# Performance work log

Hardware: AMD Instinct MI355X
Metric: run time of the kernel (lower is better)

The kernel has to match this reference:

```python
import jax, jax.numpy as jnp
import numpy as np

K = 16  # number of neighbors (self excluded), matches init k
NUM_CLASSES = 100


def setup_inputs() -> dict:
    key = jax.random.key(0)
    kx, ky = jax.random.split(key)
    N, D = 8192, 256
    x = jax.random.normal(kx, (N, D), dtype=jnp.float32)
    y = jax.random.randint(ky, (N,), 0, NUM_CLASSES, dtype=jnp.int64)
    return {"x": x, "y": y}


def _knn_loss(x, y):
    N = x.shape[0]
    k = min(K, N - 1)
    # Pairwise squared Euclidean distances via Gram trick: [N, N]
    sq_norms = jnp.sum(x * x, axis=1)
    sq = sq_norms[:, None] + sq_norms[None, :] - 2.0 * (x @ x.T)
    sq = jnp.maximum(sq, 0.0)
    eye = jnp.eye(N, dtype=bool)
    # Keep sqrt grad-safe on the (excluded) diagonal by placing a dummy 1.0 there.
    d = jnp.sqrt(jnp.where(eye, 1.0, sq))  # [N, N] Euclidean distances

    # k nearest neighbors excluding self (BallTree query k+1 then drop col 0).
    d_for_knn = jnp.where(eye, jnp.inf, d)
    _, nn_idx = jax.lax.top_k(-d_for_knn, k)  # [N, k] indices of smallest distances

    # distances = exp(-d); denominator sums over all j != i.
    exp_d = jnp.where(eye, 0.0, jnp.exp(-d))
    denom = jnp.sum(exp_d, axis=1)  # [N]

    # log(exp(-d_in) / denom_i) = -d_in - log(denom_i)
    nn_d = jnp.take_along_axis(d, nn_idx, axis=1)          # [N, k]
    log_p = -nn_d - jnp.log(denom)[:, None]                 # [N, k]

    # Only neighbors with matching label contribute; rows with none are skipped.
    match = (y[nn_idx] == y[:, None]).astype(x.dtype)       # [N, k]
    cnt = jnp.sum(match, axis=1)                            # [N]
    row_mean = jnp.where(cnt > 0, jnp.sum(log_p * match, axis=1) / jnp.maximum(cnt, 1.0), 0.0)
    return -jnp.sum(row_mean) / N


def reference(x, y):
    return _knn_loss(x, y)
```

## Files before the change

kernel.cpp:

```cpp
#include <hip/hip_runtime.h>
#include <hip/hip_fp16.h>


typedef __attribute__((ext_vector_type(8))) short s8v;
typedef __attribute__((ext_vector_type(4))) float f32x4;

#define NROW 8192
#define NK   256
#define SAMPN 512
#define TAUR  6
#define PSLOT 2

template <bool B> struct BoolC { static constexpr bool value = B; };

#define OFF_DNP  0
#define OFF_NRM  262144
#define OFF_TAU  294912
#define OFF_XB   327680
#define OFF_SAMP 4521984
#define OFF_PASS 4521984
#define PASS_BYTES (NROW * 512 * 4)

__device__ __forceinline__ unsigned short f2bf(float f) {
  unsigned u = __float_as_uint(f);
  return (unsigned short)((u + 0x7FFFu + ((u >> 16) & 1u)) >> 16);
}

__device__ __forceinline__ void gld16(const void* g, void* l) {
  __builtin_amdgcn_global_load_lds(
      (const __attribute__((address_space(1))) unsigned int*)g,
      (__attribute__((address_space(3))) unsigned int*)l, 16, 0, 0);
}

__device__ __forceinline__ unsigned umin32(unsigned a, unsigned b) { return a < b ? a : b; }

__global__ __launch_bounds__(256) void k_prep(const float* __restrict__ x,
                                              unsigned short* __restrict__ xb,
                                              float* __restrict__ nrm) {
  const int w = threadIdx.x >> 6, l = threadIdx.x & 63;
  const int r = blockIdx.x * 4 + w;
  const float4 xv = *reinterpret_cast<const float4*>(x + r * NK + l * 4);
  float ns = xv.x * xv.x + xv.y * xv.y + xv.z * xv.z + xv.w * xv.w;
  ns += __shfl_xor(ns, 1);  ns += __shfl_xor(ns, 2);  ns += __shfl_xor(ns, 4);
  ns += __shfl_xor(ns, 8);  ns += __shfl_xor(ns, 16); ns += __shfl_xor(ns, 32);
  if (l == 0) nrm[r] = ns;
  ushort4 bv;
  bv.x = f2bf(xv.x); bv.y = f2bf(xv.y); bv.z = f2bf(xv.z); bv.w = f2bf(xv.w);
  const int gs = (l >> 1) ^ (r & 7);
  *reinterpret_cast<ushort4*>(xb + r * NK + gs * 8 + (l & 1) * 4) = bv;
}

__global__ __launch_bounds__(512) void k_samp(const unsigned short* __restrict__ xb,
                                              const float* __restrict__ nrm,
                                              unsigned short* __restrict__ samp) {
  __shared__ __align__(16) unsigned short Bl[64 * NK];
  __shared__ float ncs[64];
  const int tid = threadIdx.x;
  const int w = tid >> 6, l = tid & 63, l15 = l & 15, l4 = l >> 4;
  const int rb = blockIdx.x >> 3, ss = blockIdx.x & 7;
  const int rowbase = rb * 128 + (w >> 1) * 32;
  const int wcol = (w & 1) * 32;

  #pragma unroll
  for (int jj = 0; jj < 4; ++jj) {
    const int unit = jj * 512 + tid;
    const int sc = unit >> 5, gsl = unit & 31;
    const int s = ss * 64 + sc;
    const int jrow = s * 16 + (s & 7);
    gld16(xb + jrow * NK + gsl * 8, &Bl[unit * 8]);
  }
  if (tid < 64) {
    const int s = ss * 64 + tid;
    ncs[tid] = nrm[s * 16 + (s & 7)];
  }

  s8v A[2][8];
  #pragma unroll
  for (int rf = 0; rf < 2; ++rf) {
    const int rr = rowbase + rf * 16 + l15;
    #pragma unroll
    for (int kf = 0; kf < 8; ++kf) {
      const int g = ((kf << 2) | l4) ^ (rr & 7);
      A[rf][kf] = *reinterpret_cast<const s8v*>(xb + rr * NK + g * 8);
    }
  }
  float nr[2][4];
  #pragma unroll
  for (int rf = 0; rf < 2; ++rf)
    #pragma unroll
    for (int q = 0; q < 4; ++q) nr[rf][q] = nrm[rowbase + rf * 16 + l4 * 4 + q];

  __syncthreads();
  f32x4 acc[2][2];
  #pragma unroll
  for (int rf = 0; rf < 2; ++rf) {
    f32x4 z = {0.f, 0.f, 0.f, 0.f};
    acc[rf][0] = z; acc[rf][1] = z;
  }
  #pragma unroll
  for (int kf = 0; kf < 8; ++kf) {
    const int gs = ((kf << 2) | l4) ^ (l15 & 7);
    const s8v b0 = *reinterpret_cast<const s8v*>(&Bl[(wcol + l15) * NK + gs * 8]);
    const s8v b1 = *reinterpret_cast<const s8v*>(&Bl[(wcol + 16 + l15) * NK + gs * 8]);
    #pragma unroll
    for (int rf = 0; rf < 2; ++rf) {
      acc[rf][0] = __builtin_amdgcn_mfma_f32_16x16x32_bf16(A[rf][kf], b0, acc[rf][0], 0, 0, 0);
      acc[rf][1] = __builtin_amdgcn_mfma_f32_16x16x32_bf16(A[rf][kf], b1, acc[rf][1], 0, 0, 0);
    }
  }
  #pragma unroll
  for (int rf = 0; rf < 2; ++rf)
    #pragma unroll
    for (int cf = 0; cf < 2; ++cf) {
      const int scol = ss * 64 + wcol + cf * 16 + l15;
      const int jcol = scol * 16 + (scol & 7);
      const float nc = ncs[wcol + cf * 16 + l15];
      #pragma unroll
      for (int q = 0; q < 4; ++q) {
        const int rowg = rowbase + rf * 16 + l4 * 4 + q;
        const float sq = fmaxf(fmaf(acc[rf][cf][q], -2.0f, nr[rf][q] + nc), 0.0f);
        const float dd = __builtin_amdgcn_sqrtf(sq);
        unsigned short d16 = __half_as_ushort(__float2half(dd));
        if (jcol == rowg) d16 = 0xFFFFu;
        samp[rowg * SAMPN + scol] = d16;
      }
    }
}

__global__ __launch_bounds__(256) void k_tau(const unsigned short* __restrict__ samp,
                                             unsigned* __restrict__ tauk) {
  const int w = threadIdx.x >> 6, l = threadIdx.x & 63;
  const int r = blockIdx.x * 4 + w;
  const uint4 pa = *reinterpret_cast<const uint4*>(samp + r * SAMPN + l * 8);
  unsigned v[8];
  v[0] = pa.x & 0xFFFFu; v[1] = pa.x >> 16; v[2] = pa.y & 0xFFFFu; v[3] = pa.y >> 16;
  v[4] = pa.z & 0xFFFFu; v[5] = pa.z >> 16; v[6] = pa.w & 0xFFFFu; v[7] = pa.w >> 16;
  unsigned m = 0;
  for (int pp = 0; pp < TAUR; ++pp) {
    unsigned lm = v[0];
    #pragma unroll
    for (int j = 1; j < 8; ++j) lm = umin32(lm, v[j]);
    m = lm;
    m = umin32(m, __shfl_xor(m, 1));  m = umin32(m, __shfl_xor(m, 2));
    m = umin32(m, __shfl_xor(m, 4));  m = umin32(m, __shfl_xor(m, 8));
    m = umin32(m, __shfl_xor(m, 16)); m = umin32(m, __shfl_xor(m, 32));
    const unsigned long long bal = __ballot(lm == m);
    const int owner = (int)__ffsll(bal) - 1;
    if (l == owner) {
      bool f = false;
      #pragma unroll
      for (int j = 0; j < 8; ++j)
        if (!f && v[j] == m) { v[j] = 0xFFFFFFFFu; f = true; }
    }
  }
  if (l == 0) tauk[r] = m;
}

__global__ __launch_bounds__(512) void k_main(const unsigned short* __restrict__ xb,
                                              const float* __restrict__ nrm,
                                              const unsigned* __restrict__ tauk,
                                              float* __restrict__ dnp,
                                              unsigned* __restrict__ pass) {
  __shared__ __align__(16) unsigned short Bl[2][64 * NK];
  __shared__ float ncs[2][64];
  __shared__ float dpart[128];
  const int tid = threadIdx.x;
  const int w = tid >> 6, l = tid & 63, l15 = l & 15, l4 = l >> 4;
  const int rb = blockIdx.x >> 3, cs = blockIdx.x & 7;
  const int rowbase = rb * 128 + (w >> 1) * 32;
  const int wcol = (w & 1) * 32;
  const int colslice = cs * 1024;
  const unsigned long long ltm = (1ull << l) - 1ull;
  const unsigned long long sub = 0xFFFFull << (l4 * 16);

  if (tid < 128) dpart[tid] = 0.0f;

  s8v A[2][8];
  #pragma unroll
  for (int rf = 0; rf < 2; ++rf) {
    const int rr = rowbase + rf * 16 + l15;
    #pragma unroll
    for (int kf = 0; kf < 8; ++kf) {
      const int g = ((kf << 2) | l4) ^ (rr & 7);
      A[rf][kf] = *reinterpret_cast<const s8v*>(xb + rr * NK + g * 8);
    }
  }
  float nr[2][4], tk2[2][4], dn[2][4];
  #pragma unroll
  for (int rf = 0; rf < 2; ++rf)
    #pragma unroll
    for (int q = 0; q < 4; ++q) {
      const int rowg = rowbase + rf * 16 + l4 * 4 + q;
      nr[rf][q] = nrm[rowg];
      const float tw = __half2float(__ushort_as_half((unsigned short)(tauk[rowg] + 1u)));
      tk2[rf][q] = tw * tw;
      dn[rf][q] = 0.0f;
    }

  auto stage = [&](int buf, int t) {
    const unsigned short* src = xb + (colslice + t * 64) * NK;
    #pragma unroll
    for (int jj = 0; jj < 4; ++jj)
      gld16(src + (jj * 512 + tid) * 8, &Bl[buf][(jj * 512 + w * 64) * 8]);
    if (tid < 64) ncs[buf][tid] = nrm[colslice + t * 64 + tid];
  };

  const int tdiag = rb * 2 - cs * 16;

  stage(0, 0);
  for (int t = 0; t < 16; ++t) {
    const int cur = t & 1;
    __syncthreads();
    if (t + 1 < 16) stage(cur ^ 1, t + 1);
    const int cbase = colslice + t * 64;
    f32x4 acc[2][2];
    #pragma unroll
    for (int rf = 0; rf < 2; ++rf) {
      f32x4 z = {0.f, 0.f, 0.f, 0.f};
      acc[rf][0] = z; acc[rf][1] = z;
    }
    #pragma unroll
    for (int kf = 0; kf < 8; ++kf) {
      const int gs = ((kf << 2) | l4) ^ (l15 & 7);
      const s8v b0 = *reinterpret_cast<const s8v*>(&Bl[cur][(wcol + l15) * NK + gs * 8]);
      const s8v b1 = *reinterpret_cast<const s8v*>(&Bl[cur][(wcol + 16 + l15) * NK + gs * 8]);
      #pragma unroll
      for (int rf = 0; rf < 2; ++rf) {
        acc[rf][0] = __builtin_amdgcn_mfma_f32_16x16x32_bf16(A[rf][kf], b0, acc[rf][0], 0, 0, 0);
        acc[rf][1] = __builtin_amdgcn_mfma_f32_16x16x32_bf16(A[rf][kf], b1, acc[rf][1], 0, 0, 0);
      }
    }
    const float nc0 = ncs[cur][wcol + l15];
    const float nc1 = ncs[cur][wcol + 16 + l15];
    const int colg0 = cbase + wcol + l15;
    const int colg1 = colg0 + 16;
    const int gt4 = (cs * 16 + t) * 4;
    auto epi = [&](auto dgc) {
      constexpr bool DG = decltype(dgc)::value;
      #pragma unroll
      for (int rf = 0; rf < 2; ++rf)
        #pragma unroll
        for (int q = 0; q < 4; ++q) {
          const int rowg = rowbase + rf * 16 + l4 * 4 + q;
          float sq0 = fmaf(acc[rf][0][q], -2.0f, nr[rf][q] + nc0);
          float sq1 = fmaf(acc[rf][1][q], -2.0f, nr[rf][q] + nc1);
          if (DG) { sq0 = fmaxf(sq0, 0.0f); sq1 = fmaxf(sq1, 0.0f); }
          const float d0 = __builtin_amdgcn_sqrtf(sq0);
          const float d1 = __builtin_amdgcn_sqrtf(sq1);
          float e0 = __expf(-d0), e1 = __expf(-d1);
          bool p0 = sq0 < tk2[rf][q];
          bool p1 = sq1 < tk2[rf][q];
          if (DG) {
            const bool nd0 = (rowg != colg0), nd1 = (rowg != colg1);
            e0 = nd0 ? e0 : 0.0f;  e1 = nd1 ? e1 : 0.0f;
            p0 = p0 && nd0;  p1 = p1 && nd1;
          }
          dn[rf][q] += e0 + e1;
          const unsigned long long m0 = __ballot(p0);
          const unsigned long long m1 = __ballot(p1);
          if ((m0 | m1) != 0ull) {
            const int r0 = __popcll(m0 & sub & ltm);
            const int r1 = __popcll(m1 & sub & ltm);
            if (p0 && r0 < PSLOT) {
              const unsigned d16 = __half_as_ushort(__float2half(d0));
              pass[rowg * 512 + gt4 + r0] = (d16 << 16) | (unsigned)colg0;
            }
            if (p1 && r1 < PSLOT) {
              const unsigned d16 = __half_as_ushort(__float2half(d1));
              pass[rowg * 512 + gt4 + 2 + r1] = (d16 << 16) | (unsigned)colg1;
            }
          }
        }
    };
    if (t == tdiag || t == tdiag + 1) epi(BoolC<true>{});
    else                              epi(BoolC<false>{});
  }
  #pragma unroll
  for (int rf = 0; rf < 2; ++rf)
    #pragma unroll
    for (int q = 0; q < 4; ++q) {
      float vs = dn[rf][q];
      vs += __shfl_xor(vs, 1); vs += __shfl_xor(vs, 2);
      vs += __shfl_xor(vs, 4); vs += __shfl_xor(vs, 8);
      if (l15 == 0) atomicAdd(&dpart[(w >> 1) * 32 + rf * 16 + l4 * 4 + q], vs);
    }
  __syncthreads();
  if (tid < 128) dnp[(rb * 128 + tid) * 8 + cs] = dpart[tid];
}

__global__ __launch_bounds__(256) void k_fin(const unsigned* __restrict__ pass,
                                             const float* __restrict__ dnp,
                                             const int* __restrict__ y,
                                             float* __restrict__ out) {
  const int w = threadIdx.x >> 6, l = threadIdx.x & 63;
  const int r = blockIdx.x * 4 + w;
  unsigned kk[8];
  const uint4 pa = *reinterpret_cast<const uint4*>(pass + r * 512 + l * 8);
  const uint4 pb = *reinterpret_cast<const uint4*>(pass + r * 512 + l * 8 + 4);
  kk[0] = pa.x; kk[1] = pa.y; kk[2] = pa.z; kk[3] = pa.w;
  kk[4] = pb.x; kk[5] = pb.y; kk[6] = pb.z; kk[7] = pb.w;
  unsigned myKey = 0xFFFFFFFFu;
  for (int pp = 0; pp < 16; ++pp) {
    unsigned lm = kk[0];
    #pragma unroll
    for (int j = 1; j < 8; ++j) lm = umin32(lm, kk[j]);
    unsigned m = lm;
    m = umin32(m, __shfl_xor(m, 1));  m = umin32(m, __shfl_xor(m, 2));
    m = umin32(m, __shfl_xor(m, 4));  m = umin32(m, __shfl_xor(m, 8));
    m = umin32(m, __shfl_xor(m, 16)); m = umin32(m, __shfl_xor(m, 32));
    const unsigned long long bal = __ballot(lm == m);
    const int owner = (int)__ffsll(bal) - 1;
    if (l == owner) {
      bool f = false;
      #pragma unroll
      for (int j = 0; j < 8; ++j)
        if (!f && kk[j] == m) { kk[j] = 0xFFFFFFFFu; f = true; }
    }
    if (l == pp) myKey = m;
  }
  float den = 0.0f;
  #pragma unroll
  for (int cs = 0; cs < 8; ++cs) den += dnp[r * 8 + cs];
  const float logden = __logf(den);
  float contrib = 0.0f, cmf = 0.0f;
  if (l < 16 && myKey != 0xFFFFFFFFu) {
    const int col = (int)(myKey & 0x1FFFu);
    const float dd = __half2float(__ushort_as_half((unsigned short)(myKey >> 16)));
    if (y[col] == y[r]) { contrib = -dd - logden; cmf = 1.0f; }
  }
  contrib += __shfl_xor(contrib, 1);  contrib += __shfl_xor(contrib, 2);
  contrib += __shfl_xor(contrib, 4);  contrib += __shfl_xor(contrib, 8);
  contrib += __shfl_xor(contrib, 16); contrib += __shfl_xor(contrib, 32);
  cmf += __shfl_xor(cmf, 1);  cmf += __shfl_xor(cmf, 2);
  cmf += __shfl_xor(cmf, 4);  cmf += __shfl_xor(cmf, 8);
  cmf += __shfl_xor(cmf, 16); cmf += __shfl_xor(cmf, 32);
  if (l == 0 && cmf > 0.0f)
    atomicAdd(out, (contrib / cmf) * (-1.0f / 8192.0f));
}

extern "C" void kernel_launch(void* const* d_in, const int* in_sizes, int n_in,
                              void* d_out, int out_size, void* d_ws, size_t ws_size,
                              hipStream_t stream) {
  const float* x = (const float*)d_in[0];
  const int* y = (const int*)d_in[1];
  float* out = (float*)d_out;
  char* ws = (char*)d_ws;

  float*          dnp  = (float*)(ws + OFF_DNP);
  float*          nrm  = (float*)(ws + OFF_NRM);
  unsigned*       tauk = (unsigned*)(ws + OFF_TAU);
  unsigned short* xb   = (unsigned short*)(ws + OFF_XB);
  unsigned short* samp = (unsigned short*)(ws + OFF_SAMP);
  unsigned*       pass = (unsigned*)(ws + OFF_PASS);

  k_prep<<<2048, 256, 0, stream>>>(x, xb, nrm);
  k_samp<<<512,  512, 0, stream>>>(xb, nrm, samp);
  k_tau <<<2048, 256, 0, stream>>>(samp, tauk);
  hipMemsetAsync(pass, 0xFF, PASS_BYTES, stream);
  hipMemsetAsync(d_out, 0, sizeof(float), stream);
  k_main<<<512,  512, 0, stream>>>(xb, nrm, tauk, dnp, pass);
  k_fin <<<2048, 256, 0, stream>>>(pass, dnp, y, out);
}
```

Before: 133.6 us.

## Retile main kernel to 256-thread blocks over 32-column tiles with 16 column slices

The main distance kernel moves from 512-thread blocks over 1024-column slices to 256-thread blocks over 512-column slices, doubling the grid. Each wave now covers all 32 columns of a tile, so the per-block LDS tile halves and launch bounds request 4 blocks per CU to raise occupancy. Candidate slots are reassigned: a running per-row count across pairs of tiles packs up to 4 candidates per 64-column group, replacing the fixed 2 slots per 16-column half. Denominator partials grow to 16 per row, so the workspace offsets and the final reduction change to match. A-fragment reuse per block is lower, since each wave now loads B for all its columns.

```diff
diff --git a/kernel.cpp b/kernel.cpp
--- a/kernel.cpp
+++ b/kernel.cpp
@@ -9,16 +9,15 @@
 #define NK   256
 #define SAMPN 512
 #define TAUR  6
-#define PSLOT 2
 
 template <bool B> struct BoolC { static constexpr bool value = B; };
 
 #define OFF_DNP  0
-#define OFF_NRM  262144
-#define OFF_TAU  294912
-#define OFF_XB   327680
-#define OFF_SAMP 4521984
-#define OFF_PASS 4521984
+#define OFF_NRM  524288
+#define OFF_TAU  557056
+#define OFF_XB   589824
+#define OFF_SAMP 4784128
+#define OFF_PASS 4784128
 #define PASS_BYTES (NROW * 512 * 4)
 
 __device__ __forceinline__ unsigned short f2bf(float f) {
@@ -156,20 +155,19 @@
   if (l == 0) tauk[r] = m;
 }
 
-__global__ __launch_bounds__(512) void k_main(const unsigned short* __restrict__ xb,
-                                              const float* __restrict__ nrm,
-                                              const unsigned* __restrict__ tauk,
-                                              float* __restrict__ dnp,
-                                              unsigned* __restrict__ pass) {
-  __shared__ __align__(16) unsigned short Bl[2][64 * NK];
-  __shared__ float ncs[2][64];
+__global__ __launch_bounds__(256, 4) void k_main(const unsigned short* __restrict__ xb,
+                                                 const float* __restrict__ nrm,
+                                                 const unsigned* __restrict__ tauk,
+                                                 float* __restrict__ dnp,
+                                                 unsigned* __restrict__ pass) {
+  __shared__ __align__(16) unsigned short Bl[2][32 * NK];
+  __shared__ float ncs[2][32];
   __shared__ float dpart[128];
   const int tid = threadIdx.x;
   const int w = tid >> 6, l = tid & 63, l15 = l & 15, l4 = l >> 4;
-  const int rb = blockIdx.x >> 3, cs = blockIdx.x & 7;
-  const int rowbase = rb * 128 + (w >> 1) * 32;
-  const int wcol = (w & 1) * 32;
-  const int colslice = cs * 1024;
+  const int rb = blockIdx.x >> 4, cs = blockIdx.x & 15;
+  const int rowbase = rb * 128 + w * 32;
+  const int colslice = cs * 512;
   const unsigned long long ltm = (1ull << l) - 1ull;
   const unsigned long long sub = 0xFFFFull << (l4 * 16);
 
@@ -186,6 +184,7 @@
     }
   }
   float nr[2][4], tk2[2][4], dn[2][4];
+  unsigned pcnt[2][4];
   #pragma unroll
   for (int rf = 0; rf < 2; ++rf)
     #pragma unroll
@@ -195,24 +194,25 @@
       const float tw = __half2float(__ushort_as_half((unsigned short)(tauk[rowg] + 1u)));
       tk2[rf][q] = tw * tw;
       dn[rf][q] = 0.0f;
+      pcnt[rf][q] = 0u;
     }
 
   auto stage = [&](int buf, int t) {
-    const unsigned short* src = xb + (colslice + t * 64) * NK;
+    const unsigned short* src = xb + (colslice + t * 32) * NK;
     #pragma unroll
     for (int jj = 0; jj < 4; ++jj)
-      gld16(src + (jj * 512 + tid) * 8, &Bl[buf][(jj * 512 + w * 64) * 8]);
-    if (tid < 64) ncs[buf][tid] = nrm[colslice + t * 64 + tid];
+      gld16(src + (jj * 256 + tid) * 8, &Bl[buf][(jj * 256 + tid) * 8]);
+    if (tid < 32) ncs[buf][tid] = nrm[colslice + t * 32 + tid];
   };
 
-  const int tdiag = rb * 2 - cs * 16;
+  const int tdw = rb * 4 + w - cs * 16;
 
   stage(0, 0);
   for (int t = 0; t < 16; ++t) {
     const int cur = t & 1;
     __syncthreads();
     if (t + 1 < 16) stage(cur ^ 1, t + 1);
-    const int cbase = colslice + t * 64;
+    const int cbase = colslice + t * 32;
     f32x4 acc[2][2];
     #pragma unroll
     for (int rf = 0; rf < 2; ++rf) {
@@ -222,19 +222,20 @@
     #pragma unroll
     for (int kf = 0; kf < 8; ++kf) {
       const int gs = ((kf << 2) | l4) ^ (l15 & 7);
-      const s8v b0 = *reinterpret_cast<const s8v*>(&Bl[cur][(wcol + l15) * NK + gs * 8]);
-      const s8v b1 = *reinterpret_cast<const s8v*>(&Bl[cur][(wcol + 16 + l15) * NK + gs * 8]);
+      const s8v b0 = *reinterpret_cast<const s8v*>(&Bl[cur][l15 * NK + gs * 8]);
+      const s8v b1 = *reinterpret_cast<const s8v*>(&Bl[cur][(16 + l15) * NK + gs * 8]);
       #pragma unroll
       for (int rf = 0; rf < 2; ++rf) {
         acc[rf][0] = __builtin_amdgcn_mfma_f32_16x16x32_bf16(A[rf][kf], b0, acc[rf][0], 0, 0, 0);
         acc[rf][1] = __builtin_amdgcn_mfma_f32_16x16x32_bf16(A[rf][kf], b1, acc[rf][1], 0, 0, 0);
       }
     }
-    const float nc0 = ncs[cur][wcol + l15];
-    const float nc1 = ncs[cur][wcol + 16 + l15];
-    const int colg0 = cbase + wcol + l15;
+    const float nc0 = ncs[cur][l15];
+    const float nc1 = ncs[cur][16 + l15];
+    const int colg0 = cbase + l15;
     const int colg1 = colg0 + 16;
-    const int gt4 = (cs * 16 + t) * 4;
+    const unsigned gp4 = (unsigned)(((cs * 16 + t) >> 1) * 4);
+    const bool odd = (t & 1) != 0;
     auto epi = [&](auto dgc) {
       constexpr bool DG = decltype(dgc)::value;
       #pragma unroll
@@ -258,22 +259,23 @@
           dn[rf][q] += e0 + e1;
           const unsigned long long m0 = __ballot(p0);
           const unsigned long long m1 = __ballot(p1);
-          if ((m0 | m1) != 0ull) {
-            const int r0 = __popcll(m0 & sub & ltm);
-            const int r1 = __popcll(m1 & sub & ltm);
-            if (p0 && r0 < PSLOT) {
-              const unsigned d16 = __half_as_ushort(__float2half(d0));
-              pass[rowg * 512 + gt4 + r0] = (d16 << 16) | (unsigned)colg0;
-            }
-            if (p1 && r1 < PSLOT) {
-              const unsigned d16 = __half_as_ushort(__float2half(d1));
-              pass[rowg * 512 + gt4 + 2 + r1] = (d16 << 16) | (unsigned)colg1;
-            }
+          const unsigned c0 = (unsigned)__popcll(m0 & sub);
+          const unsigned base = pcnt[rf][q];
+          const unsigned r0 = base + (unsigned)__popcll(m0 & sub & ltm);
+          const unsigned r1 = base + c0 + (unsigned)__popcll(m1 & sub & ltm);
+          if (p0 && r0 < 4u) {
+            const unsigned d16 = __half_as_ushort(__float2half(d0));
+            pass[rowg * 512 + gp4 + r0] = (d16 << 16) | (unsigned)colg0;
           }
+          if (p1 && r1 < 4u) {
+            const unsigned d16 = __half_as_ushort(__float2half(d1));
+            pass[rowg * 512 + gp4 + r1] = (d16 << 16) | (unsigned)colg1;
+          }
+          pcnt[rf][q] = odd ? 0u : base + c0 + (unsigned)__popcll(m1 & sub);
         }
     };
-    if (t == tdiag || t == tdiag + 1) epi(BoolC<true>{});
-    else                              epi(BoolC<false>{});
+    if (t == tdw) epi(BoolC<true>{});
+    else          epi(BoolC<false>{});
   }
   #pragma unroll
   for (int rf = 0; rf < 2; ++rf)
@@ -282,10 +284,10 @@
       float vs = dn[rf][q];
       vs += __shfl_xor(vs, 1); vs += __shfl_xor(vs, 2);
       vs += __shfl_xor(vs, 4); vs += __shfl_xor(vs, 8);
-      if (l15 == 0) atomicAdd(&dpart[(w >> 1) * 32 + rf * 16 + l4 * 4 + q], vs);
+      if (l15 == 0) atomicAdd(&dpart[w * 32 + rf * 16 + l4 * 4 + q], vs);
     }
   __syncthreads();
-  if (tid < 128) dnp[(rb * 128 + tid) * 8 + cs] = dpart[tid];
+  if (tid < 128) dnp[(rb * 128 + tid) * 16 + cs] = dpart[tid];
 }
 
 __global__ __launch_bounds__(256) void k_fin(const unsigned* __restrict__ pass,
@@ -320,7 +322,7 @@
   }
   float den = 0.0f;
   #pragma unroll
-  for (int cs = 0; cs < 8; ++cs) den += dnp[r * 8 + cs];
+  for (int cs = 0; cs < 16; ++cs) den += dnp[r * 16 + cs];
   const float logden = __logf(den);
   float contrib = 0.0f, cmf = 0.0f;
   if (l < 16 && myKey != 0xFFFFFFFFu) {
@@ -358,6 +360,6 @@
   k_tau <<<2048, 256, 0, stream>>>(samp, tauk);
   hipMemsetAsync(pass, 0xFF, PASS_BYTES, stream);
   hipMemsetAsync(d_out, 0, sizeof(float), stream);
-  k_main<<<512,  512, 0, stream>>>(xb, nrm, tauk, dnp, pass);
+  k_main<<<1024, 256, 0, stream>>>(xb, nrm, tauk, dnp, pass);
   k_fin <<<2048, 256, 0, stream>>>(pass, dnp, y, out);
 }
```

Measured after the change: 205.5 us. 53.8% more time.
